# Performance work log

Measured on AMD Instinct MI355X. Metric: run time of the kernel, lower is better.

The kernel has to match this reference:

```python
import jax, jax.numpy as jnp
import numpy as np

N = 100_000        # num nodes
E = 1_600_000      # num edges (self-loops appended in reference)
IN_DIM = 128
OUT_DIM = 128
NUM_HEAD = 8
D_HEAD = OUT_DIM // NUM_HEAD
NEG_SLOPE = 0.2
EPS = 1e-10


def setup_inputs() -> dict:
    key = jax.random.key(0)
    k1, k2, k3, k4, k5 = jax.random.split(key, 5)
    x = jax.random.normal(k1, (N, IN_DIM), dtype=jnp.float32)
    edge_list = jax.random.randint(k2, (E, 2), 0, N, dtype=jnp.int32)
    edge_weight = jax.random.uniform(k3, (E,), dtype=jnp.float32)
    # nn.Linear(input_dim, output_dim) params
    W = jax.random.normal(k4, (IN_DIM, OUT_DIM), dtype=jnp.float32) / np.sqrt(IN_DIM).astype(np.float32)
    b = jnp.zeros((OUT_DIM,), dtype=jnp.float32)
    # query: (num_head, 2*output_dim/num_head), kaiming-uniform-ish init
    query = jax.random.normal(k5, (NUM_HEAD, 2 * D_HEAD), dtype=jnp.float32) * 0.1
    return {"x": x, "edge_list": edge_list, "edge_weight": edge_weight,
            "W": W, "b": b, "query": query}


def reference(x, edge_list, edge_weight, W, b, query):
    # --- message ---
    self_idx = jnp.arange(N, dtype=edge_list.dtype)
    node_in = jnp.concatenate([edge_list[:, 0], self_idx])   # [E+N]
    node_out = jnp.concatenate([edge_list[:, 1], self_idx])  # [E+N]
    ew = jnp.concatenate([edge_weight, jnp.ones((N,), edge_weight.dtype)])[:, None]  # [E+N,1]

    hidden = x @ W + b                                        # [N, OUT_DIM]
    h_in = hidden[node_in]                                    # [E+N, OUT_DIM]
    h_out = hidden[node_out]                                  # [E+N, OUT_DIM]

    # torch: stack(..., dim=-1).view(-1, num_head, 2*d_head) -> interleaved layout
    key_ = jnp.stack([h_in, h_out], axis=-1).reshape(-1, NUM_HEAD, 2 * D_HEAD)
    w = jnp.einsum('hd,nhd->nh', query, key_)                 # [E+N, H]
    w = jax.nn.leaky_relu(w, NEG_SLOPE)

    seg_max = jax.ops.segment_max(w, node_out, num_segments=N)  # [N, H]
    w = w - seg_max[node_out]
    att = jnp.exp(w) * ew                                     # [E+N, H]

    counts = jax.ops.segment_sum(jnp.ones((node_out.shape[0],), att.dtype),
                                 node_out, num_segments=N)[:, None]  # [N,1] (>=1: self-loops)
    norm = jax.ops.segment_sum(att, node_out, num_segments=N) / counts  # scatter_mean
    att = att / (norm[node_out] + EPS)

    value = h_in.reshape(-1, NUM_HEAD, D_HEAD)
    message = (att[..., None] * value).reshape(-1, OUT_DIM)   # [E+N, OUT_DIM]

    # --- aggregate: scatter_mean over node_out ---
    update = jax.ops.segment_sum(message, node_out, num_segments=N) / counts

    # --- combine: relu activation, no batch norm ---
    return jax.nn.relu(update)
```

## Files before the change

kernel.cpp:

```cpp
#include <hip/hip_runtime.h>

#define NH 8
#define DH 16
#define OD 128
#define NCH 256
#define NPB 256
#define ECAP 5120

typedef __attribute__((ext_vector_type(8))) short bf16x8;
typedef __attribute__((ext_vector_type(4))) float f32x4;

__device__ inline unsigned int f2bf(float f) {
    unsigned int u = __float_as_uint(f);
    return (u + 0x7fffu + ((u >> 16) & 1u)) >> 16;
}


__global__ __launch_bounds__(256) void binhist_kernel(const int2* __restrict__ el,
                                                      int* __restrict__ cnt,
                                                      int E, int total, int CH, int NB) {
    __shared__ int lh[512];
    int t = threadIdx.x, c = blockIdx.x;
    for (int i = t; i < NB; i += 256) lh[i] = 0;
    __syncthreads();
    int beg = c * CH, end = min(total, beg + CH);
    for (int i = beg + t; i < end; i += 256) {
        int dst = (i < E) ? el[i].y : (i - E);
        atomicAdd(&lh[dst >> 8], 1);
    }
    __syncthreads();
    for (int i = t; i < NB; i += 256) cnt[i * NCH + c] = lh[i];
}

__global__ __launch_bounds__(1024) void scan1_kernel(const int* __restrict__ counts,
                                                     int* __restrict__ offsets,
                                                     int* __restrict__ bsums, int n) {
    __shared__ int tmp[1024];
    int t = threadIdx.x;
    int gid = blockIdx.x * 1024 + t;
    int v = (gid < n) ? counts[gid] : 0;
    tmp[t] = v;
    __syncthreads();
    int val = v;
    for (int off = 1; off < 1024; off <<= 1) {
        int add = (t >= off) ? tmp[t - off] : 0;
        __syncthreads();
        val += add;
        tmp[t] = val;
        __syncthreads();
    }
    if (gid < n) offsets[gid] = val - v;
    if (t == 1023) bsums[blockIdx.x] = val;
}

__global__ __launch_bounds__(1024) void scan2_kernel(int* __restrict__ bsums, int nb) {
    __shared__ int tmp[1024];
    int t = threadIdx.x;
    int v = (t < nb) ? bsums[t] : 0;
    tmp[t] = v;
    __syncthreads();
    int val = v;
    for (int off = 1; off < 1024; off <<= 1) {
        int add = (t >= off) ? tmp[t - off] : 0;
        __syncthreads();
        val += add;
        tmp[t] = val;
        __syncthreads();
    }
    if (t < nb) bsums[t] = val - v;
}

__global__ __launch_bounds__(1024) void scan3b_kernel(int* __restrict__ S,
                                                      const int* __restrict__ bsums,
                                                      const int* __restrict__ cnt, int n) {
    int gid = blockIdx.x * 1024 + threadIdx.x;
    if (gid < n) {
        int o = S[gid] + bsums[gid >> 10];
        S[gid] = o;
        if (gid == n - 1) S[n] = o + cnt[gid];
    }
}

__global__ __launch_bounds__(256) void binscatter_kernel(const int2* __restrict__ el,
                                                         const float* __restrict__ ew,
                                                         const int* __restrict__ S,
                                                         int2* __restrict__ binned,
                                                         int E, int total, int CH, int NB) {
    __shared__ int lcur[512];
    int t = threadIdx.x, c = blockIdx.x;
    for (int i = t; i < NB; i += 256) lcur[i] = S[i * NCH + c];
    __syncthreads();
    int beg = c * CH, end = min(total, beg + CH);
    for (int i = beg + t; i < end; i += 256) {
        int src, dst; float w;
        if (i < E) { int2 e = el[i]; src = e.x; dst = e.y; w = ew[i]; }
        else       { src = dst = i - E; w = 1.0f; }
        int b = dst >> 8;
        int pos = atomicAdd(&lcur[b], 1);
        binned[pos] = make_int2(src | ((dst & 255) << 17), __float_as_int(w));
    }
}

__global__ __launch_bounds__(256) void binsort_kernel(const int2* __restrict__ binned,
                                                      const int* __restrict__ S,
                                                      int2* __restrict__ sedge,
                                                      int* __restrict__ offsets,
                                                      int N, int NB, int total) {
    __shared__ int2 eb[ECAP];
    __shared__ int lh[NPB];
    __shared__ int cu[NPB];
    int b = blockIdx.x, t = threadIdx.x;
    int base = S[b * NCH];
    int endb = S[(b + 1) * NCH];
    int cnt = min(endb - base, ECAP);

    for (int i = t; i < NPB; i += 256) lh[i] = 0;
    __syncthreads();
    for (int i = t; i < cnt; i += 256) {
        int2 e = binned[base + i];
        eb[i] = e;
        atomicAdd(&lh[(e.x >> 17) & 255], 1);
    }
    __syncthreads();
    if (t < 64) {
        int loc[4]; int s = 0;
#pragma unroll
        for (int j = 0; j < 4; ++j) { loc[j] = lh[t * 4 + j]; s += loc[j]; }
        int inc = s;
        for (int d = 1; d < 64; d <<= 1) {
            int o = __shfl_up(inc, d, 64);
            if (t >= d) inc += o;
        }
        int ex = inc - s;
#pragma unroll
        for (int j = 0; j < 4; ++j) { cu[t * 4 + j] = ex; ex += loc[j]; }
    }
    __syncthreads();
    int node0 = b << 8;
    for (int i = t; i < NPB; i += 256) {
        int node = node0 + i;
        if (node < N) offsets[node] = base + cu[i];
    }
    if (b == NB - 1 && t == 0) offsets[N] = total;
    __syncthreads();
    for (int i = t; i < cnt; i += 256) {
        int2 e = eb[i];
        int d = (e.x >> 17) & 255;
        int pos = atomicAdd(&cu[d], 1);
        sedge[base + pos] = make_int2(e.x & 0x1FFFF, e.y);
    }
}

__global__ __launch_bounds__(256) void gemm_proj_kernel(
        const float* __restrict__ x, const float* __restrict__ W,
        const float* __restrict__ b, const float* __restrict__ query,
        unsigned short* __restrict__ hbu, float* __restrict__ ain,
        float* __restrict__ aout, int N) {
    __shared__ unsigned short xs[64 * 136];
    __shared__ unsigned short wt[128 * 136];
    int t = threadIdx.x;
    int row0 = blockIdx.x * 64;

    {
        const float4* x4 = (const float4*)x;
#pragma unroll
        for (int i = 0; i < 8; ++i) {
            int f = t + i * 256;
            int row = f >> 5, c4 = f & 31;
            int gr = row0 + row;
            if (gr >= N) gr = N - 1;
            float4 v = x4[(size_t)gr * 32 + c4];
            unsigned int u0 = f2bf(v.x) | (f2bf(v.y) << 16);
            unsigned int u1 = f2bf(v.z) | (f2bf(v.w) << 16);
            *(uint2*)&xs[row * 136 + 4 * c4] = make_uint2(u0, u1);
        }
    }
    {
        const float4* W4 = (const float4*)W;
#pragma unroll
        for (int i = 0; i < 16; ++i) {
            int f = t + i * 256;
            int k = f & 127, c4 = f >> 7;
            float4 v = W4[k * 32 + c4];
            wt[(4 * c4 + 0) * 136 + k] = (unsigned short)f2bf(v.x);
            wt[(4 * c4 + 1) * 136 + k] = (unsigned short)f2bf(v.y);
            wt[(4 * c4 + 2) * 136 + k] = (unsigned short)f2bf(v.z);
            wt[(4 * c4 + 3) * 136 + k] = (unsigned short)f2bf(v.w);
        }
    }
    __syncthreads();

    int lane = t & 63, wv = t >> 6;
    int d = lane & 15, g = lane >> 4;
    int tbase = wv * 16;

    bf16x8 af[4];
#pragma unroll
    for (int s = 0; s < 4; ++s)
        af[s] = *(bf16x8*)&xs[(tbase + d) * 136 + s * 32 + g * 8];

    f32x4 acc[8];
#pragma unroll
    for (int c = 0; c < 8; ++c) acc[c] = (f32x4){0.f, 0.f, 0.f, 0.f};

#pragma unroll
    for (int c = 0; c < 8; ++c) {
#pragma unroll
        for (int s = 0; s < 4; ++s) {
            bf16x8 bf = *(bf16x8*)&wt[(d + 16 * c) * 136 + s * 32 + g * 8];
            acc[c] = __builtin_amdgcn_mfma_f32_16x16x32_bf16(af[s], bf, acc[c], 0, 0, 0);
        }
    }

    int rbase = row0 + tbase + g * 4;
#pragma unroll
    for (int c = 0; c < 8; ++c) {
        float bc = b[d + 16 * c];
        float2 q2 = *(const float2*)(query + c * 2 * DH + 2 * d);
#pragma unroll
        for (int j = 0; j < 4; ++j) {
            float v = acc[c][j] + bc;
            int row = rbase + j;
            if (row < N) hbu[(size_t)row * OD + d + 16 * c] = (unsigned short)f2bf(v);
            float pin = q2.x * v, pout = q2.y * v;
#pragma unroll
            for (int m = 1; m < 16; m <<= 1) {
                pin  += __shfl_xor(pin, m, 64);
                pout += __shfl_xor(pout, m, 64);
            }
            if (d == 0 && row < N) {
                ain[row * NH + c] = pin;
                aout[row * NH + c] = pout;
            }
        }
    }
}

__global__ __launch_bounds__(256) void aggregate_kernel(
        const int* __restrict__ offsets, const int2* __restrict__ sedge,
        const float* __restrict__ ain, const float* __restrict__ aout,
        const unsigned int* __restrict__ hb, float* __restrict__ out, int N) {
    int n = (blockIdx.x * blockDim.x + threadIdx.x) >> 6;
    int lane = threadIdx.x & 63;
    if (n >= N) return;
    int beg = offsets[n], end = offsets[n + 1];
    int h = lane >> 3;
    float ao = aout[n * NH + h];

    float ssum = 0.0f;
    float2 acc = make_float2(0.0f, 0.0f);
    int t = beg;
    for (; t + 1 < end; t += 2) {
        int2 e0 = sedge[t];
        int2 e1 = sedge[t + 1];
        unsigned int vv0 = hb[(size_t)e0.x * 64 + lane];
        float a0 = ain[e0.x * NH + h];
        unsigned int vv1 = hb[(size_t)e1.x * 64 + lane];
        float a1 = ain[e1.x * NH + h];
        float w0 = a0 + ao; w0 = (w0 > 0.0f) ? w0 : 0.2f * w0;
        float w1 = a1 + ao; w1 = (w1 > 0.0f) ? w1 : 0.2f * w1;
        float ex0 = __expf(w0) * __int_as_float(e0.y);
        float ex1 = __expf(w1) * __int_as_float(e1.y);
        float v00 = __uint_as_float(vv0 << 16);
        float v01 = __uint_as_float(vv0 & 0xffff0000u);
        float v10 = __uint_as_float(vv1 << 16);
        float v11 = __uint_as_float(vv1 & 0xffff0000u);
        ssum += ex0 + ex1;
        acc.x += ex0 * v00 + ex1 * v10;
        acc.y += ex0 * v01 + ex1 * v11;
    }
    if (t < end) {
        int2 e0 = sedge[t];
        unsigned int vv0 = hb[(size_t)e0.x * 64 + lane];
        float a0 = ain[e0.x * NH + h];
        float w0 = a0 + ao; w0 = (w0 > 0.0f) ? w0 : 0.2f * w0;
        float ex0 = __expf(w0) * __int_as_float(e0.y);
        ssum += ex0;
        acc.x += ex0 * __uint_as_float(vv0 << 16);
        acc.y += ex0 * __uint_as_float(vv0 & 0xffff0000u);
    }
    float c = (float)(end - beg);
    float scale = 1.0f / ((ssum / c + 1e-10f) * c);
    float o0 = acc.x * scale, o1 = acc.y * scale;
    *(float2*)(out + (size_t)n * OD + 2 * lane) =
        make_float2(o0 > 0.0f ? o0 : 0.0f, o1 > 0.0f ? o1 : 0.0f);
}

extern "C" void kernel_launch(void* const* d_in, const int* in_sizes, int n_in,
                              void* d_out, int out_size, void* d_ws, size_t ws_size,
                              hipStream_t stream) {
    const float* x     = (const float*)d_in[0];
    const int2*  el    = (const int2*)d_in[1];
    const float* ew    = (const float*)d_in[2];
    const float* W     = (const float*)d_in[3];
    const float* b     = (const float*)d_in[4];
    const float* query = (const float*)d_in[5];
    float* out = (float*)d_out;

    int N = in_sizes[0] / OD;
    int E = in_sizes[1] / 2;
    int total = E + N;
    int NB = (N + NPB - 1) / NPB;
    int CH = (total + NCH - 1) / NCH;
    int n2 = NB * NCH;

    char* ws = (char*)d_ws;
    size_t off = 0;
    auto take = [&](size_t bytes) -> void* {
        void* p = ws + off;
        off = (off + bytes + 255) & ~(size_t)255;
        return p;
    };
    unsigned int* hb = (unsigned int*)take((size_t)N * 64 * 4);
    float* ain     = (float*)take((size_t)N * NH * 4);
    float* aout    = (float*)take((size_t)N * NH * 4);
    int*   cnt     = (int*)take((size_t)n2 * 4);
    int*   S       = (int*)take((size_t)(n2 + 1) * 4);
    int*   offsets = (int*)take((size_t)(N + 1) * 4);
    int*   bsums   = (int*)take(4096);
    int2*  binned  = (int2*)take((size_t)total * 8);
    int2*  sedge   = (int2*)take((size_t)total * 8);

    binhist_kernel<<<NCH, 256, 0, stream>>>(el, cnt, E, total, CH, NB);
    int nb = (n2 + 1023) / 1024;
    scan1_kernel<<<nb, 1024, 0, stream>>>(cnt, S, bsums, n2);
    scan2_kernel<<<1, 1024, 0, stream>>>(bsums, nb);
    scan3b_kernel<<<nb, 1024, 0, stream>>>(S, bsums, cnt, n2);
    binscatter_kernel<<<NCH, 256, 0, stream>>>(el, ew, S, binned, E, total, CH, NB);
    binsort_kernel<<<NB, 256, 0, stream>>>(binned, S, sedge, offsets, N, NB, total);
    gemm_proj_kernel<<<(N + 63) / 64, 256, 0, stream>>>(
        x, W, b, query, (unsigned short*)hb, ain, aout, N);
    aggregate_kernel<<<((size_t)N * 64 + 255) / 256, 256, 0, stream>>>(
        offsets, sedge, ain, aout, hb, out, N);
}
```

Measured before the change: 213.8 us.

## Halve binsort bin size and distribute edge attention across lanes in aggregate

The binning stages now group destinations into bins of 128 nodes instead of 256, which doubles the bin count and shrinks the per-block shared edge buffer. The aggregate kernel changes so that each lane of an 8-lane head group computes the attention weight for a different edge. Weights and source indices are then broadcast with shuffles and the partial sums reduced at the end. This avoids every lane redundantly computing exp and loading ain and sedge for each edge, at the cost of extra shuffles and a serial inner loop with a break.

```diff
diff --git a/kernel.cpp b/kernel.cpp
--- a/kernel.cpp
+++ b/kernel.cpp
@@ -4,8 +4,8 @@
 #define DH 16
 #define OD 128
 #define NCH 256
-#define NPB 256
-#define ECAP 5120
+#define NPB 128
+#define ECAP 3072
 
 typedef __attribute__((ext_vector_type(8))) short bf16x8;
 typedef __attribute__((ext_vector_type(4))) float f32x4;
@@ -19,14 +19,14 @@
 __global__ __launch_bounds__(256) void binhist_kernel(const int2* __restrict__ el,
                                                       int* __restrict__ cnt,
                                                       int E, int total, int CH, int NB) {
-    __shared__ int lh[512];
+    __shared__ int lh[1024];
     int t = threadIdx.x, c = blockIdx.x;
     for (int i = t; i < NB; i += 256) lh[i] = 0;
     __syncthreads();
     int beg = c * CH, end = min(total, beg + CH);
     for (int i = beg + t; i < end; i += 256) {
         int dst = (i < E) ? el[i].y : (i - E);
-        atomicAdd(&lh[dst >> 8], 1);
+        atomicAdd(&lh[dst >> 7], 1);
     }
     __syncthreads();
     for (int i = t; i < NB; i += 256) cnt[i * NCH + c] = lh[i];
@@ -86,7 +86,7 @@
                                                          const int* __restrict__ S,
                                                          int2* __restrict__ binned,
                                                          int E, int total, int CH, int NB) {
-    __shared__ int lcur[512];
+    __shared__ int lcur[1024];
     int t = threadIdx.x, c = blockIdx.x;
     for (int i = t; i < NB; i += 256) lcur[i] = S[i * NCH + c];
     __syncthreads();
@@ -95,9 +95,9 @@
         int src, dst; float w;
         if (i < E) { int2 e = el[i]; src = e.x; dst = e.y; w = ew[i]; }
         else       { src = dst = i - E; w = 1.0f; }
-        int b = dst >> 8;
+        int b = dst >> 7;
         int pos = atomicAdd(&lcur[b], 1);
-        binned[pos] = make_int2(src | ((dst & 255) << 17), __float_as_int(w));
+        binned[pos] = make_int2(src | ((dst & 127) << 17), __float_as_int(w));
     }
 }
 
@@ -119,13 +119,13 @@
     for (int i = t; i < cnt; i += 256) {
         int2 e = binned[base + i];
         eb[i] = e;
-        atomicAdd(&lh[(e.x >> 17) & 255], 1);
+        atomicAdd(&lh[(e.x >> 17) & 127], 1);
     }
     __syncthreads();
     if (t < 64) {
-        int loc[4]; int s = 0;
-#pragma unroll
-        for (int j = 0; j < 4; ++j) { loc[j] = lh[t * 4 + j]; s += loc[j]; }
+        int loc[2]; int s = 0;
+#pragma unroll
+        for (int j = 0; j < 2; ++j) { loc[j] = lh[t * 2 + j]; s += loc[j]; }
         int inc = s;
         for (int d = 1; d < 64; d <<= 1) {
             int o = __shfl_up(inc, d, 64);
@@ -133,10 +133,10 @@
         }
         int ex = inc - s;
 #pragma unroll
-        for (int j = 0; j < 4; ++j) { cu[t * 4 + j] = ex; ex += loc[j]; }
-    }
-    __syncthreads();
-    int node0 = b << 8;
+        for (int j = 0; j < 2; ++j) { cu[t * 2 + j] = ex; ex += loc[j]; }
+    }
+    __syncthreads();
+    int node0 = b << 7;
     for (int i = t; i < NPB; i += 256) {
         int node = node0 + i;
         if (node < N) offsets[node] = base + cu[i];
@@ -145,7 +145,7 @@
     __syncthreads();
     for (int i = t; i < cnt; i += 256) {
         int2 e = eb[i];
-        int d = (e.x >> 17) & 255;
+        int d = (e.x >> 17) & 127;
         int pos = atomicAdd(&cu[d], 1);
         sedge[base + pos] = make_int2(e.x & 0x1FFFF, e.y);
     }
@@ -244,41 +244,38 @@
     int lane = threadIdx.x & 63;
     if (n >= N) return;
     int beg = offsets[n], end = offsets[n + 1];
-    int h = lane >> 3;
+    int h = lane >> 3, s = lane & 7;
+    int gbase = lane & 56;
     float ao = aout[n * NH + h];
 
     float ssum = 0.0f;
     float2 acc = make_float2(0.0f, 0.0f);
-    int t = beg;
-    for (; t + 1 < end; t += 2) {
-        int2 e0 = sedge[t];
-        int2 e1 = sedge[t + 1];
-        unsigned int vv0 = hb[(size_t)e0.x * 64 + lane];
-        float a0 = ain[e0.x * NH + h];
-        unsigned int vv1 = hb[(size_t)e1.x * 64 + lane];
-        float a1 = ain[e1.x * NH + h];
-        float w0 = a0 + ao; w0 = (w0 > 0.0f) ? w0 : 0.2f * w0;
-        float w1 = a1 + ao; w1 = (w1 > 0.0f) ? w1 : 0.2f * w1;
-        float ex0 = __expf(w0) * __int_as_float(e0.y);
-        float ex1 = __expf(w1) * __int_as_float(e1.y);
-        float v00 = __uint_as_float(vv0 << 16);
-        float v01 = __uint_as_float(vv0 & 0xffff0000u);
-        float v10 = __uint_as_float(vv1 << 16);
-        float v11 = __uint_as_float(vv1 & 0xffff0000u);
-        ssum += ex0 + ex1;
-        acc.x += ex0 * v00 + ex1 * v10;
-        acc.y += ex0 * v01 + ex1 * v11;
-    }
-    if (t < end) {
-        int2 e0 = sedge[t];
-        unsigned int vv0 = hb[(size_t)e0.x * 64 + lane];
-        float a0 = ain[e0.x * NH + h];
-        float w0 = a0 + ao; w0 = (w0 > 0.0f) ? w0 : 0.2f * w0;
-        float ex0 = __expf(w0) * __int_as_float(e0.y);
-        ssum += ex0;
-        acc.x += ex0 * __uint_as_float(vv0 << 16);
-        acc.y += ex0 * __uint_as_float(vv0 & 0xffff0000u);
-    }
+    for (int i = beg; i < end; i += 8) {
+        int idx = i + s;
+        float att = 0.0f;
+        int src = 0;
+        if (idx < end) {
+            int2 e = sedge[idx];
+            src = e.x;
+            float a = ain[src * NH + h] + ao;
+            a = (a > 0.0f) ? a : 0.2f * a;
+            att = __expf(a) * __int_as_float(e.y);
+        }
+        ssum += att;
+#pragma unroll
+        for (int ss = 0; ss < 8; ++ss) {
+            if (i + ss >= end) break;
+            float att_s = __shfl(att, gbase | ss, 64);
+            int src_s = __shfl(src, gbase | ss, 64);
+            unsigned int vv = hb[(size_t)src_s * 64 + lane];
+            acc.x += att_s * __uint_as_float(vv << 16);
+            acc.y += att_s * __uint_as_float(vv & 0xffff0000u);
+        }
+    }
+    ssum += __shfl_xor(ssum, 1, 64);
+    ssum += __shfl_xor(ssum, 2, 64);
+    ssum += __shfl_xor(ssum, 4, 64);
+
     float c = (float)(end - beg);
     float scale = 1.0f / ((ssum / c + 1e-10f) * c);
     float o0 = acc.x * scale, o1 = acc.y * scale;
```

After: 233.1 us. 1.09x slower.
